# Kernel optimization log

Hardware: AMD Instinct MI355X
Metric: run time of the kernel (lower is better)

## Reference

```python
import jax, jax.numpy as jnp
import numpy as np

K = 4
TEMPERATURE = 30.0


def setup_inputs() -> dict:
    key = jax.random.key(0)
    ks = jax.random.split(key, 6)
    B, C, H, W_sp = 32, 128, 56, 56
    Cout, kh, kw = 128, 3, 3
    Cred = max(C // 4, 1)
    x = jax.random.normal(ks[0], (B, C, H, W_sp), dtype=jnp.float32)
    # K parallel conv kernels + biases (fan-in scaled init)
    fan = C * kh * kw
    W = jax.random.normal(ks[1], (K, Cout, C, kh, kw), dtype=jnp.float32) / np.sqrt(fan)
    b = jax.random.normal(ks[2], (K, Cout), dtype=jnp.float32) * 0.01
    # attention branch: 1x1 convs == dense on pooled features
    aw1 = jax.random.normal(ks[3], (Cred, C), dtype=jnp.float32) / np.sqrt(C)
    aw2 = jax.random.normal(ks[4], (K, Cred), dtype=jnp.float32) / np.sqrt(Cred)
    return {"x": x, "W": W, "b": b, "aw1": aw1, "aw2": aw2}


def reference(x, W, b, aw1, aw2):
    # attention: global avg pool -> 1x1 conv (dense) -> relu -> 1x1 conv -> softmax(logits/T)
    pooled = jnp.mean(x, axis=(2, 3))                       # [B, C]
    h1 = jax.nn.relu(jnp.einsum('bc,rc->br', pooled, aw1))  # [B, Cred]
    logits = jnp.einsum('br,kr->bk', h1, aw2)               # [B, K]
    attn = jax.nn.softmax(logits / TEMPERATURE, axis=1)     # [B, K]

    pad = 1
    out = None
    for i in range(K):  # fixed small K, structurally distinct kernels
        yi = jax.lax.conv_general_dilated(
            x, W[i], window_strides=(1, 1), padding=[(pad, pad), (pad, pad)],
            dimension_numbers=('NCHW', 'OIHW', 'NCHW'))
        yi = yi + b[i][None, :, None, None]
        yi = yi * attn[:, i][:, None, None, None]
        out = yi if out is None else out + yi
    return out
```

## Files before the change

### kernel.cpp

```cpp
#include <hip/hip_runtime.h>
#include <hip/hip_bf16.h>
#include <stdint.h>

typedef __bf16 bf16x8 __attribute__((ext_vector_type(8)));
typedef float  f32x4  __attribute__((ext_vector_type(4)));
typedef unsigned short u16x8 __attribute__((ext_vector_type(8)));

#define NB 32
#define NC 128
#define NH 56
#define NW 56
#define NK 4
#define NCO 128
#define NCR 32
#define NHW 3136
#define TEMPER 30.0f

#define WS_ATTN   0u
#define WS_BC     4096u
#define WS_ROWSUM 65536u
#define WS_WC     1048576u
#define WS_XT     10485760u

__global__ void xt_kernel(const float* __restrict__ x, __hip_bfloat16* __restrict__ xt,
                          float* __restrict__ rowsum) {
  __shared__ float lds[58 * 133];
  int xcd = blockIdx.x & 7;
  int j   = blockIdx.x >> 3;
  int b   = xcd * 4 + j / 58;
  int hp  = j % 58;
  int blk = b * 58 + hp;
  int h = hp - 1;
  bool hin = (h >= 0) && (h < NH);
  int tid = threadIdx.x;
  if (hin) {
    const float* xrow = x + ((size_t)b * NC) * NHW + (size_t)h * NW;
    for (int i = tid; i < 128 * 14; i += 256) {
      int c = i / 14;
      int w4 = (i - c * 14) * 4;
      float4 v = *(const float4*)(xrow + (size_t)c * NHW + w4);
      int base = (w4 + 1) * 133 + c;
      lds[base]         = v.x;
      lds[base + 133]   = v.y;
      lds[base + 2*133] = v.z;
      lds[base + 3*133] = v.w;
    }
  }
  __syncthreads();
  __hip_bfloat16* orow = xt + (size_t)blk * (58 * 128);
  for (int i = tid; i < 58 * 16; i += 256) {
    int wp = i >> 4;
    int cg = (i & 15) << 3;
    u16x8 o;
    if (!hin || wp == 0 || wp == 57) {
      o = (u16x8)0;
    } else {
      const float* src = lds + wp * 133 + cg;
      #pragma unroll
      for (int jx = 0; jx < 8; ++jx) {
        union { __hip_bfloat16 b; unsigned short u; } cv;
        cv.b = __float2bfloat16(src[jx]);
        o[jx] = cv.u;
      }
    }
    *(u16x8*)(orow + wp * 128 + cg) = o;
  }
  if (hin && tid < 128) {
    float s = 0.f;
    #pragma unroll 8
    for (int wp = 1; wp <= 56; ++wp) s += lds[wp * 133 + tid];
    rowsum[(size_t)blk * 128 + tid] = s;
  }
}

__global__ void attn_kernel(const float* __restrict__ rowsum, const float* __restrict__ aw1,
                            const float* __restrict__ aw2, const float* __restrict__ bias,
                            float* __restrict__ attn, float* __restrict__ bc_out) {
  int b = blockIdx.x;
  __shared__ float sp[NC], h1[NCR], at[NK];
  int t = threadIdx.x;
  if (t < NC) {
    float s = 0.f;
    for (int hp = 1; hp <= 56; ++hp) s += rowsum[((size_t)b * 58 + hp) * 128 + t];
    sp[t] = s * (1.0f / (float)NHW);
  }
  __syncthreads();
  if (t < NCR) {
    float s = 0.f;
    for (int c = 0; c < NC; ++c) s += aw1[t*NC + c] * sp[c];
    h1[t] = s > 0.f ? s : 0.f;
  }
  __syncthreads();
  if (t == 0) {
    float lg[NK], mx = -1e30f;
    for (int k = 0; k < NK; ++k) {
      float s = 0.f;
      for (int r = 0; r < NCR; ++r) s += aw2[k*NCR + r] * h1[r];
      lg[k] = s * (1.0f/TEMPER);
      mx = fmaxf(mx, lg[k]);
    }
    float den = 0.f, e[NK];
    for (int k = 0; k < NK; ++k) { e[k] = expf(lg[k]-mx); den += e[k]; }
    float inv = 1.0f/den;
    for (int k = 0; k < NK; ++k) { at[k] = e[k]*inv; attn[b*NK+k] = at[k]; }
  }
  __syncthreads();
  if (t < NCO) {
    float s = 0.f;
    for (int k = 0; k < NK; ++k) s += at[k] * bias[k*NCO + t];
    bc_out[b*NCO + t] = s;
  }
}

__global__ void combine_kernel(const float* __restrict__ W, const float* __restrict__ attn,
                               __hip_bfloat16* __restrict__ wc) {
  int gid = blockIdx.x;
  int bg  = gid >> 6;
  int tcell = (gid & 63) * 256 + threadIdx.x;
  int co = tcell >> 7, ci = tcell & 127;
  float w[4][9];
  const float* wp = W + ((size_t)co * 128 + ci) * 9;
  #pragma unroll
  for (int k = 0; k < 4; ++k)
    #pragma unroll
    for (int j = 0; j < 9; ++j)
      w[k][j] = wp[(size_t)k * 147456 + j];
  for (int b = bg * 8; b < bg * 8 + 8; ++b) {
    float a0 = attn[b*4+0], a1 = attn[b*4+1], a2 = attn[b*4+2], a3 = attn[b*4+3];
    #pragma unroll
    for (int j = 0; j < 9; ++j) {
      float v = a0*w[0][j] + a1*w[1][j] + a2*w[2][j] + a3*w[3][j];
      wc[(((size_t)b*9 + j) * 128 + co) * 128 + ci] = __float2bfloat16(v);
    }
  }
}

#define RS 2368
#define CS 40
#define BBUF (3072*8)
#define ABUF (1536*8)

#define GLOAD16(src, dst) \
  __builtin_amdgcn_global_load_lds( \
    (const __attribute__((address_space(1))) unsigned int*)(src), \
    (__attribute__((address_space(3))) unsigned int*)(dst), 16, 0, 0)

__global__ __launch_bounds__(512, 2) void conv_kernel(
    const unsigned short* __restrict__ xt,
    const unsigned short* __restrict__ wc,
    const float* __restrict__ bc,
    float* __restrict__ out) {
  __shared__ __align__(16) unsigned short lds_a[2*ABUF];
  __shared__ __align__(16) unsigned short lds_b[2*BBUF];
  const int tid  = threadIdx.x;
  const int lane = tid & 63;
  const int wv   = tid >> 6;
  const int wm   = wv >> 2;
  const int wn   = wv & 3;
  const int bid  = blockIdx.x;
  const int xcd  = bid & 7;
  const int jj   = bid >> 3;
  const int b    = xcd*4 + jj/7;
  const int r0   = (jj % 7) * 8;
  const int li   = lane & 15;
  const int kg   = lane >> 4;

  int srcB[6];
  #pragma unroll
  for (int i = 0; i < 6; ++i) {
    int q = i*512 + tid;
    int r = q / 296;
    int sl = q - r*296;
    int col = sl / 5;
    int part = sl - col*5;
    int rc = r  > 9  ? 9  : r;
    int cl = col > 57 ? 57 : col;
    int pc = part > 3 ? 3 : part;
    srcB[i] = ((r0 + rc)*58 + cl)*128 + pc*8;
  }
  int srcA[3];
  #pragma unroll
  for (int i = 0; i < 3; ++i) {
    int c = i*512 + tid;
    int kwl  = c >> 9;
    int co   = (c & 511) >> 2;
    int part = c & 3;
    srcA[i] = (kwl*128 + co)*128 + part*8;
  }

  int xoff[7];
  #pragma unroll
  for (int f = 0; f < 7; ++f) {
    int pos = wn*112 + f*16 + li;
    int rB = pos / 56;
    int cB = pos - rB*56;
    xoff[f] = rB*RS + cB*CS + kg*8;
  }
  const int aRead = (wm*64 + li)*32 + kg*8;

  const f32x4 vzero = {0.f, 0.f, 0.f, 0.f};
  f32x4 acc[4][7];
  #pragma unroll
  for (int mo = 0; mo < 4; ++mo)
    #pragma unroll
    for (int f = 0; f < 7; ++f) acc[mo][f] = vzero;

  const unsigned short* xtg = xt + (size_t)b*(58*58*128);
  const unsigned short* wcg = wc + (size_t)b*(9*128*128);

  #define STAGE_A(bufidx, ccn, khn) do { \
    unsigned short* dbase = lds_a + (bufidx)*ABUF + wv*512; \
    _Pragma("unroll") \
    for (int i = 0; i < 3; ++i) \
      GLOAD16(wcg + (khn)*49152 + srcA[i] + (ccn)*32, dbase + i*4096); \
  } while (0)

  #define STAGE_B(bufidx, ccn) do { \
    unsigned short* dbase = lds_b + (bufidx)*BBUF + wv*512; \
    _Pragma("unroll") \
    for (int i = 0; i < 6; ++i) \
      GLOAD16(xtg + srcB[i] + (ccn)*32, dbase + i*4096); \
  } while (0)

  #define LOADFRAG(AF, BF, pa, pb, kwl, kh) do { \
    _Pragma("unroll") \
    for (int mo = 0; mo < 4; ++mo) \
      AF[mo] = *(const bf16x8*)((pa) + (kwl)*4096 + aRead + mo*512); \
    _Pragma("unroll") \
    for (int f = 0; f < 7; ++f) \
      BF[f] = *(const bf16x8*)((pb) + xoff[f] + (kh)*RS + (kwl)*CS); \
  } while (0)

  #define DOMFMA(AF, BF) do { \
    __builtin_amdgcn_s_setprio(1); \
    _Pragma("unroll") \
    for (int mo = 0; mo < 4; ++mo) \
      _Pragma("unroll") \
      for (int f = 0; f < 7; ++f) \
        acc[mo][f] = __builtin_amdgcn_mfma_f32_16x16x32_bf16(AF[mo], BF[f], acc[mo][f], 0, 0, 0); \
    __builtin_amdgcn_s_setprio(0); \
  } while (0)

  #define STEP(s, cc, kh, VM) do { \
    if ((s) < 11) STAGE_A(((s)+1)&1, ((s)+1)/3, ((s)+1)%3); \
    if ((kh) == 0 && (cc) < 3) STAGE_B(((cc)+1)&1, (cc)+1); \
    asm volatile("s_waitcnt vmcnt(" #VM ")" ::: "memory"); \
    __builtin_amdgcn_s_barrier(); \
    { \
      const unsigned short* pa = lds_a + ((s)&1)*ABUF; \
      const unsigned short* pb = lds_b + ((cc)&1)*BBUF; \
      bf16x8 afE[4], bfE[7], afO[4], bfO[7]; \
      LOADFRAG(afE, bfE, pa, pb, 0, kh); \
      LOADFRAG(afO, bfO, pa, pb, 1, kh); \
      DOMFMA(afE, bfE); \
      LOADFRAG(afE, bfE, pa, pb, 2, kh); \
      DOMFMA(afO, bfO); \
      DOMFMA(afE, bfE); \
    } \
    __builtin_amdgcn_s_barrier(); \
  } while (0)

  STAGE_A(0, 0, 0);
  STAGE_B(0, 0);

  STEP(0,  0, 0, 9);
  STEP(1,  0, 1, 9);
  STEP(2,  0, 2, 3);
  STEP(3,  1, 0, 9);
  STEP(4,  1, 1, 9);
  STEP(5,  1, 2, 3);
  STEP(6,  2, 0, 9);
  STEP(7,  2, 1, 9);
  STEP(8,  2, 2, 3);
  STEP(9,  3, 0, 3);
  STEP(10, 3, 1, 3);
  STEP(11, 3, 2, 0);

  float* ob = out + (size_t)b*NCO*NHW;
  #pragma unroll
  for (int mo = 0; mo < 4; ++mo) {
    #pragma unroll
    for (int rg = 0; rg < 4; ++rg) {
      const int co = wm*64 + mo*16 + kg*4 + rg;
      const float bv = bc[b*NCO + co];
      float* orow = ob + (size_t)co*NHW;
      #pragma unroll
      for (int f = 0; f < 7; ++f) {
        int pos = wn*112 + f*16 + li;
        int rB = pos / 56;
        int cB = pos - rB*56;
        orow[(r0 + rB)*56 + cB] = acc[mo][f][rg] + bv;
      }
    }
  }
}

extern "C" void kernel_launch(void* const* d_in, const int* in_sizes, int n_in,
                              void* d_out, int out_size, void* d_ws, size_t ws_size,
                              hipStream_t stream) {
  const float* x   = (const float*)d_in[0];
  const float* W   = (const float*)d_in[1];
  const float* bia = (const float*)d_in[2];
  const float* aw1 = (const float*)d_in[3];
  const float* aw2 = (const float*)d_in[4];
  float* out = (float*)d_out;
  char* ws = (char*)d_ws;
  float* attn   = (float*)(ws + WS_ATTN);
  float* bcm    = (float*)(ws + WS_BC);
  float* rowsum = (float*)(ws + WS_ROWSUM);
  __hip_bfloat16* wc = (__hip_bfloat16*)(ws + WS_WC);
  __hip_bfloat16* xt = (__hip_bfloat16*)(ws + WS_XT);

  xt_kernel<<<NB*58, 256, 0, stream>>>(x, xt, rowsum);
  attn_kernel<<<NB, 128, 0, stream>>>(rowsum, aw1, aw2, bia, attn, bcm);
  combine_kernel<<<256, 256, 0, stream>>>(W, attn, wc);
  conv_kernel<<<224, 512, 0, stream>>>((const unsigned short*)xt,
                                       (const unsigned short*)wc, bcm, out);
}
```

Before: 68.31 us.

## Replace direct global-to-LDS loads with register-staged prefetch and LDS writes

Swaps the global_load_lds direct-to-LDS async copies for ordinary vector global loads into registers, issued before the compute of each step and written to the other LDS buffer afterward, between two __syncthreads. It also simplifies the fragment loading to a straightforward per-kw loop instead of the interleaved even/odd double-buffered fragments. The aim is to let the compiler schedule the loads and waits itself rather than relying on hand-tuned vmcnt counts. In exchange it adds staging registers (36 VGPRs) under a 512x2 launch bound, an extra LDS write pass, and loses the explicit fragment prefetch overlap.

```diff
diff --git a/kernel.cpp b/kernel.cpp
--- a/kernel.cpp
+++ b/kernel.cpp
@@ -5,6 +5,7 @@
 typedef __bf16 bf16x8 __attribute__((ext_vector_type(8)));
 typedef float  f32x4  __attribute__((ext_vector_type(4)));
 typedef unsigned short u16x8 __attribute__((ext_vector_type(8)));
+typedef unsigned int   u32x4 __attribute__((ext_vector_type(4)));
 
 #define NB 32
 #define NC 128
@@ -140,11 +141,6 @@
 #define BBUF (3072*8)
 #define ABUF (1536*8)
 
-#define GLOAD16(src, dst) \
-  __builtin_amdgcn_global_load_lds( \
-    (const __attribute__((address_space(1))) unsigned int*)(src), \
-    (__attribute__((address_space(3))) unsigned int*)(dst), 16, 0, 0)
-
 __global__ __launch_bounds__(512, 2) void conv_kernel(
     const unsigned short* __restrict__ xt,
     const unsigned short* __restrict__ wc,
@@ -208,73 +204,82 @@
   const unsigned short* xtg = xt + (size_t)b*(58*58*128);
   const unsigned short* wcg = wc + (size_t)b*(9*128*128);
 
-  #define STAGE_A(bufidx, ccn, khn) do { \
-    unsigned short* dbase = lds_a + (bufidx)*ABUF + wv*512; \
+  u32x4 aST[3], bST[6];
+
+  #define LOAD_A(ccn, khn) do { \
     _Pragma("unroll") \
     for (int i = 0; i < 3; ++i) \
-      GLOAD16(wcg + (khn)*49152 + srcA[i] + (ccn)*32, dbase + i*4096); \
-  } while (0)
-
-  #define STAGE_B(bufidx, ccn) do { \
-    unsigned short* dbase = lds_b + (bufidx)*BBUF + wv*512; \
+      aST[i] = *(const u32x4*)(wcg + (khn)*49152 + srcA[i] + (ccn)*32); \
+  } while (0)
+
+  #define LOAD_B(ccn) do { \
     _Pragma("unroll") \
     for (int i = 0; i < 6; ++i) \
-      GLOAD16(xtg + srcB[i] + (ccn)*32, dbase + i*4096); \
-  } while (0)
-
-  #define LOADFRAG(AF, BF, pa, pb, kwl, kh) do { \
-    _Pragma("unroll") \
-    for (int mo = 0; mo < 4; ++mo) \
-      AF[mo] = *(const bf16x8*)((pa) + (kwl)*4096 + aRead + mo*512); \
-    _Pragma("unroll") \
-    for (int f = 0; f < 7; ++f) \
-      BF[f] = *(const bf16x8*)((pb) + xoff[f] + (kh)*RS + (kwl)*CS); \
-  } while (0)
-
-  #define DOMFMA(AF, BF) do { \
-    __builtin_amdgcn_s_setprio(1); \
-    _Pragma("unroll") \
-    for (int mo = 0; mo < 4; ++mo) \
+      bST[i] = *(const u32x4*)(xtg + srcB[i] + (ccn)*32); \
+  } while (0)
+
+  #define WRITE_A(bufidx) do { \
+    _Pragma("unroll") \
+    for (int i = 0; i < 3; ++i) \
+      *(u32x4*)(lds_a + (bufidx)*ABUF + (i*512 + tid)*8) = aST[i]; \
+  } while (0)
+
+  #define WRITE_B(bufidx) do { \
+    _Pragma("unroll") \
+    for (int i = 0; i < 6; ++i) \
+      *(u32x4*)(lds_b + (bufidx)*BBUF + (i*512 + tid)*8) = bST[i]; \
+  } while (0)
+
+  #define COMPUTE(s, cc, kh) do { \
+    const unsigned short* pa = lds_a + ((s)&1)*ABUF; \
+    const unsigned short* pb = lds_b + ((cc)&1)*BBUF; \
+    _Pragma("unroll") \
+    for (int kwl = 0; kwl < 3; ++kwl) { \
+      bf16x8 af[4], bf[7]; \
+      _Pragma("unroll") \
+      for (int mo = 0; mo < 4; ++mo) \
+        af[mo] = *(const bf16x8*)(pa + kwl*4096 + aRead + mo*512); \
       _Pragma("unroll") \
       for (int f = 0; f < 7; ++f) \
-        acc[mo][f] = __builtin_amdgcn_mfma_f32_16x16x32_bf16(AF[mo], BF[f], acc[mo][f], 0, 0, 0); \
-    __builtin_amdgcn_s_setprio(0); \
-  } while (0)
-
-  #define STEP(s, cc, kh, VM) do { \
-    if ((s) < 11) STAGE_A(((s)+1)&1, ((s)+1)/3, ((s)+1)%3); \
-    if ((kh) == 0 && (cc) < 3) STAGE_B(((cc)+1)&1, (cc)+1); \
-    asm volatile("s_waitcnt vmcnt(" #VM ")" ::: "memory"); \
-    __builtin_amdgcn_s_barrier(); \
-    { \
-      const unsigned short* pa = lds_a + ((s)&1)*ABUF; \
-      const unsigned short* pb = lds_b + ((cc)&1)*BBUF; \
-      bf16x8 afE[4], bfE[7], afO[4], bfO[7]; \
-      LOADFRAG(afE, bfE, pa, pb, 0, kh); \
-      LOADFRAG(afO, bfO, pa, pb, 1, kh); \
-      DOMFMA(afE, bfE); \
-      LOADFRAG(afE, bfE, pa, pb, 2, kh); \
-      DOMFMA(afO, bfO); \
-      DOMFMA(afE, bfE); \
+        bf[f] = *(const bf16x8*)(pb + xoff[f] + (kh)*RS + kwl*CS); \
+      __builtin_amdgcn_s_setprio(1); \
+      _Pragma("unroll") \
+      for (int mo = 0; mo < 4; ++mo) \
+        _Pragma("unroll") \
+        for (int f = 0; f < 7; ++f) \
+          acc[mo][f] = __builtin_amdgcn_mfma_f32_16x16x32_bf16(af[mo], bf[f], acc[mo][f], 0, 0, 0); \
+      __builtin_amdgcn_s_setprio(0); \
     } \
-    __builtin_amdgcn_s_barrier(); \
-  } while (0)
-
-  STAGE_A(0, 0, 0);
-  STAGE_B(0, 0);
-
-  STEP(0,  0, 0, 9);
-  STEP(1,  0, 1, 9);
-  STEP(2,  0, 2, 3);
-  STEP(3,  1, 0, 9);
-  STEP(4,  1, 1, 9);
-  STEP(5,  1, 2, 3);
-  STEP(6,  2, 0, 9);
-  STEP(7,  2, 1, 9);
-  STEP(8,  2, 2, 3);
-  STEP(9,  3, 0, 3);
-  STEP(10, 3, 1, 3);
-  STEP(11, 3, 2, 0);
+  } while (0)
+
+  #define STEP(s, cc, kh) do { \
+    if ((s) < 11) LOAD_A(((s)+1)/3, ((s)+1)%3); \
+    if ((kh) == 0 && (cc) < 3) LOAD_B((cc)+1); \
+    COMPUTE(s, cc, kh); \
+    __syncthreads(); \
+    if ((s) < 11) WRITE_A(((s)+1)&1); \
+    if ((kh) == 0 && (cc) < 3) WRITE_B(((cc)+1)&1); \
+    __syncthreads(); \
+  } while (0)
+
+  LOAD_A(0, 0);
+  LOAD_B(0);
+  WRITE_A(0);
+  WRITE_B(0);
+  __syncthreads();
+
+  STEP(0,  0, 0);
+  STEP(1,  0, 1);
+  STEP(2,  0, 2);
+  STEP(3,  1, 0);
+  STEP(4,  1, 1);
+  STEP(5,  1, 2);
+  STEP(6,  2, 0);
+  STEP(7,  2, 1);
+  STEP(8,  2, 2);
+  STEP(9,  3, 0);
+  STEP(10, 3, 1);
+  STEP(11, 3, 2);
 
   float* ob = out + (size_t)b*NCO*NHW;
   #pragma unroll
```

Result: no change. 67.41 us (-1.3%).
